# Optimization experiments

Measured on AMD Instinct MI355X. Metric: run time of the kernel, lower is better.

Reference implementation:

```python
import jax, jax.numpy as jnp
import numpy as np

EMBED_DIM = 64
CODEBOOK_SIZE = 2048
COMMITMENT_COST = 1.0


def setup_inputs() -> dict:
    key = jax.random.key(0)
    k1, k2 = jax.random.split(key)
    inputs = jax.random.normal(k1, (32, 2048, EMBED_DIM), dtype=jnp.float32)
    embeddings = jax.random.normal(k2, (EMBED_DIM, CODEBOOK_SIZE), dtype=jnp.float32)
    return {"inputs": inputs, "embeddings": embeddings}


def reference(inputs, embeddings):
    # inference path (training=False): deterministic argmin quantization.
    D = embeddings.shape[0]
    K = embeddings.shape[1]
    flat = inputs.reshape(-1, D)                       # [N, D]
    similarity = flat @ embeddings                     # [N, K]
    distances = (jnp.sum(flat * flat, axis=1, keepdims=True)
                 - 2.0 * similarity
                 + jnp.sum(embeddings * embeddings, axis=0, keepdims=True))
    # gumbel layer with temperature 0 / eval mode -> argmax(-dist) == argmin(dist)
    flat_indices = jnp.argmax(-distances, axis=1)      # [N]
    encodings = jax.nn.one_hot(flat_indices, K, dtype=jnp.float32)  # [N, K]
    encoding_indices = flat_indices.reshape(inputs.shape[:-1])      # [B, T]
    quantized = jnp.take(embeddings.T, encoding_indices, axis=0)    # [B, T, D]
    e_latent_loss = jnp.mean(jnp.square(jax.lax.stop_gradient(quantized) - inputs))
    loss = e_latent_loss * COMMITMENT_COST
    return quantized, encodings, encoding_indices, loss
```

## Files before the change

### kernel.cpp

```cpp
#include <hip/hip_runtime.h>

#define N_ROWS 65536
#define DDIM   64
#define KCODES 2048
#define NB     128
#define CHUNK  256
#define NCHUNK (KCODES / CHUNK)
#define TAU    0.05f

#define Q_OFF    ((size_t)0)
#define ENC_OFF  ((size_t)N_ROWS * DDIM)
#define IDX_OFF  (ENC_OFF + (size_t)N_ROWS * KCODES)
#define LOSS_OFF (IDX_OFF + (size_t)N_ROWS)
#define INV_ND (1.0f / ((float)N_ROWS * (float)DDIM))

#define WS_ESQ_OFF   (524288)
#define WS_FLAGS_OFF (532480)

typedef __attribute__((ext_vector_type(8))) short short8;
typedef __attribute__((ext_vector_type(4))) float f32x4;

__device__ __forceinline__ unsigned short f2bf(float f) {
    unsigned u = __float_as_uint(f);
    u += 0x7FFFu + ((u >> 16) & 1u);
    return (unsigned short)(u >> 16);
}
__device__ __forceinline__ float bf2f(unsigned short h) {
    return __uint_as_float(((unsigned)h) << 16);
}

__global__ void vq_prep(const float* __restrict__ emb, char* __restrict__ ws,
                        float* __restrict__ out) {
    int t = blockIdx.x * 256 + threadIdx.x;
    int code = t & (KCODES - 1);
    int d    = t >> 11;
    float v = emb[(size_t)d * KCODES + code];
    unsigned short hi = f2bf(v);
    unsigned short lo = f2bf(v - bf2f(hi));
    int ch = code >> 8;
    int lc = code & 255;
    int kk = d ^ ((code & 7) << 3);
    short* base = (short*)ws + (size_t)ch * 32768 + lc * 64 + kk;
    base[0]     = (short)hi;
    base[16384] = (short)lo;
    if (t < KCODES) {
        float s = 0.f;
        for (int dd = 0; dd < DDIM; ++dd) {
            float e = emb[(size_t)dd * KCODES + t];
            s += e * e;
        }
        ((float*)(ws + WS_ESQ_OFF))[t] = s;
    }
    if (t == 0) out[LOSS_OFF] = 0.f;
}

__launch_bounds__(256, 2)
__global__ void vq_main(const float* __restrict__ x, const float* __restrict__ emb,
                        const char* __restrict__ ws, int* __restrict__ flags,
                        float* __restrict__ out) {
    __shared__ __align__(16) short Bs[32768];
    const int tid = threadIdx.x;
    const int l = tid & 63, w = tid >> 6;
    const int q = l >> 4, c = l & 15;
    const int r0 = blockIdx.x * NB;
    const float* esq = (const float*)(ws + WS_ESQ_OFF);

    short8 ah0[2], ah1[2], al0[2], al1[2];
    #pragma unroll
    for (int rt = 0; rt < 2; ++rt) {
        int row = r0 + w * 32 + rt * 16 + c;
        const float4* xr = (const float4*)(x + (size_t)row * DDIM);
        float4 f0 = xr[q * 2],     f1 = xr[q * 2 + 1];
        float4 f2 = xr[8 + q * 2], f3 = xr[8 + q * 2 + 1];
        float a0[8] = {f0.x,f0.y,f0.z,f0.w,f1.x,f1.y,f1.z,f1.w};
        float a1[8] = {f2.x,f2.y,f2.z,f2.w,f3.x,f3.y,f3.z,f3.w};
        #pragma unroll
        for (int j = 0; j < 8; ++j) {
            unsigned short h0 = f2bf(a0[j]);
            ah0[rt][j] = (short)h0;
            al0[rt][j] = (short)f2bf(a0[j] - bf2f(h0));
            unsigned short h1 = f2bf(a1[j]);
            ah1[rt][j] = (short)h1;
            al1[rt][j] = (short)f2bf(a1[j] - bf2f(h1));
        }
    }

    float m1[8], m2[8]; int i1[8];
    #pragma unroll
    for (int s = 0; s < 8; ++s) { m1[s] = 3.4e38f; m2[s] = 3.4e38f; i1[s] = 0; }

    for (int ch = 0; ch < NCHUNK; ++ch) {
        const int kc = ch * CHUNK;
        __syncthreads();
        {
            const int4* g4 = (const int4*)(ws + (size_t)ch * 65536);
            int4* s4 = (int4*)Bs;
            #pragma unroll
            for (int i = 0; i < 16; ++i) s4[i * 256 + tid] = g4[i * 256 + tid];
        }
        __syncthreads();

        {
            float4 z = make_float4(0.f, 0.f, 0.f, 0.f);
            float* ebase = out + ENC_OFF + (size_t)r0 * KCODES + kc;
            #pragma unroll
            for (int j = 0; j < 32; ++j) {
                int s   = j * 256 + tid;
                int row = s >> 6;
                int c4  = s & 63;
                *(float4*)(ebase + (size_t)row * KCODES + (c4 << 2)) = z;
            }
        }

        const int swz = (c & 7) << 3;
        for (int t = 0; t < 16; ++t) {
            int codeL = t * 16 + c;
            const short* ph = Bs + codeL * 64;
            const short* pl = ph + 16384;
            int k0 = (q * 8) ^ swz;
            int k1 = (32 + q * 8) ^ swz;
            short8 bh0 = *(const short8*)(ph + k0);
            short8 bh1 = *(const short8*)(ph + k1);
            short8 bl0 = *(const short8*)(pl + k0);
            short8 bl1 = *(const short8*)(pl + k1);
            int   kidx = kc + t * 16 + c;
            float eq   = esq[kidx];
            #pragma unroll
            for (int rt = 0; rt < 2; ++rt) {
                f32x4 acc = {0.f, 0.f, 0.f, 0.f};
                acc = __builtin_amdgcn_mfma_f32_16x16x32_bf16(ah0[rt], bh0, acc, 0, 0, 0);
                acc = __builtin_amdgcn_mfma_f32_16x16x32_bf16(ah1[rt], bh1, acc, 0, 0, 0);
                acc = __builtin_amdgcn_mfma_f32_16x16x32_bf16(ah0[rt], bl0, acc, 0, 0, 0);
                acc = __builtin_amdgcn_mfma_f32_16x16x32_bf16(ah1[rt], bl1, acc, 0, 0, 0);
                acc = __builtin_amdgcn_mfma_f32_16x16x32_bf16(al0[rt], bh0, acc, 0, 0, 0);
                acc = __builtin_amdgcn_mfma_f32_16x16x32_bf16(al1[rt], bh1, acc, 0, 0, 0);
                #pragma unroll
                for (int g = 0; g < 4; ++g) {
                    float dist = fmaf(-2.f, acc[g], eq);
                    int s = rt * 4 + g;
                    bool better = dist < m1[s];
                    m2[s] = fminf(m2[s], fmaxf(m1[s], dist));
                    m1[s] = fminf(m1[s], dist);
                    i1[s] = better ? kidx : i1[s];
                }
            }
        }
    }

    __syncthreads();
    float* red  = (float*)Bs;
    int*   indS = (int*)(red + 6144);
    float* lred = red + 6144 + 128;

    #pragma unroll
    for (int rt = 0; rt < 2; ++rt)
        #pragma unroll
        for (int g = 0; g < 4; ++g) {
            int lrow = w * 32 + rt * 16 + q * 4 + g;
            float* p = red + (size_t)(lrow * 16 + c) * 3;
            p[0] = m1[rt * 4 + g];
            p[1] = (float)i1[rt * 4 + g];
            p[2] = m2[rt * 4 + g];
        }
    __syncthreads();

    if (tid < NB) {
        int row = tid;
        const float* p = red + (size_t)row * 48;
        float gm1 = 3.4e38f; int gi1 = 0x7fffffff; int wt = -1;
        for (int t = 0; t < 16; ++t) {
            float v  = p[t * 3 + 0];
            int   iv = (int)p[t * 3 + 1];
            if (v < gm1 || (v == gm1 && iv < gi1)) { gm1 = v; gi1 = iv; wt = t; }
        }
        float gm2 = 3.4e38f;
        for (int t = 0; t < 16; ++t) {
            float cand = (t == wt) ? p[t * 3 + 2] : p[t * 3 + 0];
            gm2 = fminf(gm2, cand);
        }
        int gr = r0 + row;
        out[IDX_OFF + gr] = (float)gi1;
        flags[gr] = (gm2 - gm1 < TAU) ? 1 : 0;
        indS[row] = gi1;
        out[ENC_OFF + (size_t)gr * KCODES + gi1] = 1.0f;
    }
    __syncthreads();

    float lpart = 0.f;
    for (int i = tid; i < NB * (DDIM / 4); i += 256) {
        int row = i >> 4;
        int d4  = (i & 15) << 2;
        int idx = indS[row];
        int gr  = r0 + row;
        float4 qv;
        qv.x = emb[(size_t)(d4 + 0) * KCODES + idx];
        qv.y = emb[(size_t)(d4 + 1) * KCODES + idx];
        qv.z = emb[(size_t)(d4 + 2) * KCODES + idx];
        qv.w = emb[(size_t)(d4 + 3) * KCODES + idx];
        *(float4*)(out + Q_OFF + (size_t)gr * DDIM + d4) = qv;
        float4 xv = *(const float4*)(x + (size_t)gr * DDIM + d4);
        float dx = qv.x - xv.x, dy = qv.y - xv.y, dz = qv.z - xv.z, dw = qv.w - xv.w;
        lpart += dx * dx + dy * dy + dz * dz + dw * dw;
    }
    #pragma unroll
    for (int o = 32; o > 0; o >>= 1) lpart += __shfl_down(lpart, o);
    if ((tid & 63) == 0) lred[tid >> 6] = lpart;
    __syncthreads();
    if (tid == 0)
        atomicAdd(out + LOSS_OFF, (lred[0] + lred[1] + lred[2] + lred[3]) * INV_ND);
}

__global__ void vq_refine(const float* __restrict__ x, const float* __restrict__ emb,
                          const int* __restrict__ flags, float* __restrict__ out) {
    const int lane = threadIdx.x & 63;
    const int wid  = threadIdx.x >> 6;
    for (int rr = 0; rr < 8; ++rr) {
        int row = (blockIdx.x * 4 + wid) * 8 + rr;
        if (flags[row] == 0) continue;
        const float* xr = x + (size_t)row * DDIM;
        double best = 1e300; int bidx = 0x7fffffff;
        for (int k = lane; k < KCODES; k += 64) {
            double s = 0.0, ee = 0.0;
            for (int d = 0; d < DDIM; ++d) {
                double e = (double)emb[(size_t)d * KCODES + k];
                s  = fma((double)xr[d], e, s);
                ee = fma(e, e, ee);
            }
            double dist = ee - 2.0 * s;
            if (dist < best) { best = dist; bidx = k; }
        }
        #pragma unroll
        for (int o = 32; o > 0; o >>= 1) {
            double ob = __shfl_down(best, o);
            int    oi = __shfl_down(bidx, o);
            if (ob < best || (ob == best && oi < bidx)) { best = ob; bidx = oi; }
        }
        bidx = __shfl(bidx, 0);
        int oldIdx = (int)out[IDX_OFF + row];
        if (bidx == oldIdx) continue;
        if (lane == 0) {
            out[IDX_OFF + row] = (float)bidx;
            out[ENC_OFF + (size_t)row * KCODES + oldIdx] = 0.f;
            out[ENC_OFF + (size_t)row * KCODES + bidx]   = 1.f;
        }
        float eN = emb[(size_t)lane * KCODES + bidx];
        float eO = emb[(size_t)lane * KCODES + oldIdx];
        float xv = xr[lane];
        out[Q_OFF + (size_t)row * DDIM + lane] = eN;
        float dn = eN - xv, dod = eO - xv;
        float delta = dn * dn - dod * dod;
        #pragma unroll
        for (int o = 32; o > 0; o >>= 1) delta += __shfl_down(delta, o);
        if (lane == 0) atomicAdd(out + LOSS_OFF, delta * INV_ND);
    }
}

extern "C" void kernel_launch(void* const* d_in, const int* in_sizes, int n_in,
                              void* d_out, int out_size, void* d_ws, size_t ws_size,
                              hipStream_t stream) {
    const float* x   = (const float*)d_in[0];
    const float* emb = (const float*)d_in[1];
    float* out   = (float*)d_out;
    char*  ws    = (char*)d_ws;
    int*   flags = (int*)(ws + WS_FLAGS_OFF);
    hipLaunchKernelGGL(vq_prep,   dim3(512),         dim3(256), 0, stream, emb, ws, out);
    hipLaunchKernelGGL(vq_main,   dim3(N_ROWS / NB), dim3(256), 0, stream, x, emb, ws, flags, out);
    hipLaunchKernelGGL(vq_refine, dim3(N_ROWS / 32), dim3(256), 0, stream, x, emb, flags, out);
}
```

Measured before the change: 760.6 us.

## Track top-3 distances to refine ambiguous rows with two-candidate check

The main kernel now keeps the best, second-best and third-best distances plus the second index per row. When only two codes fall within the tolerance, the flag encodes the runner-up index. The refine kernel then compares just those two codes in double precision instead of scanning all 2048 codes. This is meant to cut the cost of the full fallback scan, in exchange for more registers and extra select logic in the hot argmin loop, plus a larger shared reduction buffer.

```diff
diff --git a/kernel.cpp b/kernel.cpp
--- a/kernel.cpp
+++ b/kernel.cpp
@@ -85,9 +85,11 @@
         }
     }
 
-    float m1[8], m2[8]; int i1[8];
+    float m1[8], m2[8], m3[8]; int i1[8], i2[8];
     #pragma unroll
-    for (int s = 0; s < 8; ++s) { m1[s] = 3.4e38f; m2[s] = 3.4e38f; i1[s] = 0; }
+    for (int s = 0; s < 8; ++s) {
+        m1[s] = 3.4e38f; m2[s] = 3.4e38f; m3[s] = 3.4e38f; i1[s] = 0; i2[s] = 0;
+    }
 
     for (int ch = 0; ch < NCHUNK; ++ch) {
         const int kc = ch * CHUNK;
@@ -138,10 +140,14 @@
                 for (int g = 0; g < 4; ++g) {
                     float dist = fmaf(-2.f, acc[g], eq);
                     int s = rt * 4 + g;
-                    bool better = dist < m1[s];
-                    m2[s] = fminf(m2[s], fmaxf(m1[s], dist));
-                    m1[s] = fminf(m1[s], dist);
-                    i1[s] = better ? kidx : i1[s];
+                    bool b1 = dist < m1[s];
+                    bool b2 = dist < m2[s];
+                    bool b3 = dist < m3[s];
+                    m3[s] = b2 ? m2[s] : (b3 ? dist : m3[s]);
+                    m2[s] = b1 ? m1[s] : (b2 ? dist : m2[s]);
+                    i2[s] = b1 ? i1[s] : (b2 ? kidx : i2[s]);
+                    m1[s] = b1 ? dist : m1[s];
+                    i1[s] = b1 ? kidx : i1[s];
                 }
             }
         }
@@ -149,38 +155,49 @@
 
     __syncthreads();
     float* red  = (float*)Bs;
-    int*   indS = (int*)(red + 6144);
-    float* lred = red + 6144 + 128;
+    int*   indS = (int*)(red + 10240);
+    float* lred = red + 10240 + 128;
 
     #pragma unroll
     for (int rt = 0; rt < 2; ++rt)
         #pragma unroll
         for (int g = 0; g < 4; ++g) {
             int lrow = w * 32 + rt * 16 + q * 4 + g;
-            float* p = red + (size_t)(lrow * 16 + c) * 3;
-            p[0] = m1[rt * 4 + g];
-            p[1] = (float)i1[rt * 4 + g];
-            p[2] = m2[rt * 4 + g];
+            float* p = red + (size_t)(lrow * 16 + c) * 5;
+            int s = rt * 4 + g;
+            p[0] = m1[s];
+            p[1] = (float)i1[s];
+            p[2] = m2[s];
+            p[3] = (float)i2[s];
+            p[4] = m3[s];
         }
     __syncthreads();
 
     if (tid < NB) {
         int row = tid;
-        const float* p = red + (size_t)row * 48;
-        float gm1 = 3.4e38f; int gi1 = 0x7fffffff; int wt = -1;
+        const float* p = red + (size_t)row * 80;
+        float gm1 = 3.4e38f, gm2v = 3.4e38f, gm3 = 3.4e38f;
+        int gi1 = 0x7fffffff, gi2 = 0x7fffffff;
         for (int t = 0; t < 16; ++t) {
-            float v  = p[t * 3 + 0];
-            int   iv = (int)p[t * 3 + 1];
-            if (v < gm1 || (v == gm1 && iv < gi1)) { gm1 = v; gi1 = iv; wt = t; }
-        }
-        float gm2 = 3.4e38f;
-        for (int t = 0; t < 16; ++t) {
-            float cand = (t == wt) ? p[t * 3 + 2] : p[t * 3 + 0];
-            gm2 = fminf(gm2, cand);
+            float v1 = p[t * 5 + 0], v2 = p[t * 5 + 2], v3 = p[t * 5 + 4];
+            int   j1 = (int)p[t * 5 + 1], j2 = (int)p[t * 5 + 3];
+            if (v1 < gm1 || (v1 == gm1 && j1 < gi1)) {
+                gm3 = gm2v; gm2v = gm1; gi2 = gi1; gm1 = v1; gi1 = j1;
+            } else if (v1 < gm2v || (v1 == gm2v && j1 < gi2)) {
+                gm3 = gm2v; gm2v = v1; gi2 = j1;
+            } else if (v1 < gm3) gm3 = v1;
+            if (v2 < gm1 || (v2 == gm1 && j2 < gi1)) {
+                gm3 = gm2v; gm2v = gm1; gi2 = gi1; gm1 = v2; gi1 = j2;
+            } else if (v2 < gm2v || (v2 == gm2v && j2 < gi2)) {
+                gm3 = gm2v; gm2v = v2; gi2 = j2;
+            } else if (v2 < gm3) gm3 = v2;
+            if (v3 < gm3) gm3 = v3;
         }
         int gr = r0 + row;
         out[IDX_OFF + gr] = (float)gi1;
-        flags[gr] = (gm2 - gm1 < TAU) ? 1 : 0;
+        int f = 0;
+        if (gm2v - gm1 < TAU) f = (gm3 - gm1 < TAU) ? 1 : ((gi2 << 2) | 2);
+        flags[gr] = f;
         indS[row] = gi1;
         out[ENC_OFF + (size_t)gr * KCODES + gi1] = 1.0f;
     }
@@ -216,27 +233,48 @@
     const int wid  = threadIdx.x >> 6;
     for (int rr = 0; rr < 8; ++rr) {
         int row = (blockIdx.x * 4 + wid) * 8 + rr;
-        if (flags[row] == 0) continue;
+        int f = flags[row];
+        if (f == 0) continue;
         const float* xr = x + (size_t)row * DDIM;
-        double best = 1e300; int bidx = 0x7fffffff;
-        for (int k = lane; k < KCODES; k += 64) {
-            double s = 0.0, ee = 0.0;
-            for (int d = 0; d < DDIM; ++d) {
-                double e = (double)emb[(size_t)d * KCODES + k];
-                s  = fma((double)xr[d], e, s);
-                ee = fma(e, e, ee);
-            }
-            double dist = ee - 2.0 * s;
-            if (dist < best) { best = dist; bidx = k; }
-        }
-        #pragma unroll
-        for (int o = 32; o > 0; o >>= 1) {
-            double ob = __shfl_down(best, o);
-            int    oi = __shfl_down(bidx, o);
-            if (ob < best || (ob == best && oi < bidx)) { best = ob; bidx = oi; }
-        }
-        bidx = __shfl(bidx, 0);
         int oldIdx = (int)out[IDX_OFF + row];
+        int bidx;
+        if (f != 1) {
+            int cand = f >> 2;
+            double xd = (double)xr[lane];
+            double ea = (double)emb[(size_t)lane * KCODES + oldIdx];
+            double eb = (double)emb[(size_t)lane * KCODES + cand];
+            double sa = xd * ea, sb = xd * eb;
+            double qa = ea * ea, qb = eb * eb;
+            #pragma unroll
+            for (int o = 32; o > 0; o >>= 1) {
+                sa += __shfl_down(sa, o);
+                sb += __shfl_down(sb, o);
+                qa += __shfl_down(qa, o);
+                qb += __shfl_down(qb, o);
+            }
+            double dA = __shfl(qa - 2.0 * sa, 0);
+            double dB = __shfl(qb - 2.0 * sb, 0);
+            bidx = (dB < dA || (dB == dA && cand < oldIdx)) ? cand : oldIdx;
+        } else {
+            double best = 1e300; int bi = 0x7fffffff;
+            for (int k = lane; k < KCODES; k += 64) {
+                double s = 0.0, ee = 0.0;
+                for (int d = 0; d < DDIM; ++d) {
+                    double e = (double)emb[(size_t)d * KCODES + k];
+                    s  = fma((double)xr[d], e, s);
+                    ee = fma(e, e, ee);
+                }
+                double dist = ee - 2.0 * s;
+                if (dist < best) { best = dist; bi = k; }
+            }
+            #pragma unroll
+            for (int o = 32; o > 0; o >>= 1) {
+                double ob = __shfl_down(best, o);
+                int    oi = __shfl_down(bi, o);
+                if (ob < best || (ob == best && oi < bi)) { best = ob; bi = oi; }
+            }
+            bidx = __shfl(bi, 0);
+        }
         if (bidx == oldIdx) continue;
         if (lane == 0) {
             out[IDX_OFF + row] = (float)bidx;
```

New measurement: 708.6 us. 1.07x faster.
